# Performance work log

Hardware: AMD Instinct MI355X
Metric: run time of the kernel (lower is better)

## Reference

```python
import jax, jax.numpy as jnp
import numpy as np

N_KW, N_RT = 100000, 20000
D, H, O = 128, 128, 128
E_A, E_B, E_C = 1600000, 1600000, 320000


def setup_inputs() -> dict:
    key = jax.random.key(0)
    ks = jax.random.split(key, 32)
    inp = {
        "x_kw": jax.random.normal(ks[0], (N_KW, D), jnp.float32),
        "x_rt": jax.random.normal(ks[1], (N_RT, D), jnp.float32),
        "src_a": jax.random.randint(ks[2], (E_A,), 0, N_RT),
        "dst_a": jax.random.randint(ks[3], (E_A,), 0, N_KW),
        "src_b": jax.random.randint(ks[4], (E_B,), 0, N_KW),
        "dst_b": jax.random.randint(ks[5], (E_B,), 0, N_KW),
        "src_c": jax.random.randint(ks[6], (E_C,), 0, N_RT),
        "dst_c": jax.random.randint(ks[7], (E_C,), 0, N_RT),
    }
    # SAGEConv params per relation per layer: W_l (neighbor), b_l, W_r (root, no bias)
    i = 8
    dims = {1: (D, H), 2: (H, O)}
    for layer in (1, 2):
        din, dout = dims[layer]
        for rel in ("a", "b", "c"):
            inp[f"Wl{layer}{rel}"] = jax.random.normal(ks[i], (din, dout), jnp.float32) * 0.05; i += 1
            inp[f"bl{layer}{rel}"] = jnp.zeros((dout,), jnp.float32)
            inp[f"Wr{layer}{rel}"] = jax.random.normal(ks[i], (din, dout), jnp.float32) * 0.05; i += 1
    return inp


def _sage(x_src, x_dst, src, dst, Wl, bl, Wr):
    # PyG SAGEConv (mean aggr): lin_l(mean_j x_src[j]) + lin_r(x_dst)
    n = x_dst.shape[0]
    s = jax.ops.segment_sum(x_src[src], dst, num_segments=n)      # [n, din]
    cnt = jax.ops.segment_sum(jnp.ones_like(dst, dtype=x_src.dtype), dst, num_segments=n)
    mean = s / jnp.maximum(cnt, 1.0)[:, None]
    return mean @ Wl + bl + x_dst @ Wr


def reference(x_kw, x_rt, src_a, dst_a, src_b, dst_b, src_c, dst_c,
              Wl1a, bl1a, Wr1a, Wl1b, bl1b, Wr1b, Wl1c, bl1c, Wr1c,
              Wl2a, bl2a, Wr2a, Wl2b, bl2b, Wr2b, Wl2c, bl2c, Wr2c):
    # layer 1 (HeteroConv aggr='sum' over relations sharing a dst type)
    kw1 = (_sage(x_rt, x_kw, src_a, dst_a, Wl1a, bl1a, Wr1a)
           + _sage(x_kw, x_kw, src_b, dst_b, Wl1b, bl1b, Wr1b))
    rt1 = _sage(x_rt, x_rt, src_c, dst_c, Wl1c, bl1c, Wr1c)
    kw1 = jax.nn.relu(kw1)
    rt1 = jax.nn.relu(rt1)
    # layer 2
    kw2 = (_sage(rt1, kw1, src_a, dst_a, Wl2a, bl2a, Wr2a)
           + _sage(kw1, kw1, src_b, dst_b, Wl2b, bl2b, Wr2b))
    rt2 = _sage(rt1, rt1, src_c, dst_c, Wl2c, bl2c, Wr2c)
    return kw2, rt2
```

## Files before the change

### kernel.cpp

```cpp
#include <hip/hip_runtime.h>

typedef __attribute__((ext_vector_type(8))) short bf16x8;
typedef __attribute__((ext_vector_type(4))) float f32x4;
typedef __attribute__((ext_vector_type(2))) float f32x2;

static __device__ __forceinline__ unsigned short f2bf(float f) {
    unsigned int u = __float_as_uint(f);
    u += 0x7fffu + ((u >> 16) & 1u);
    return (unsigned short)(u >> 16);
}
static __device__ __forceinline__ float bf2f(unsigned short h) {
    return __uint_as_float(((unsigned int)h) << 16);
}

#define BSH 6
#define BUCKET 64
#define NBMAX 1600
#define CHSH 13


struct Rel {
    const int* src; const int* dst; int E; int nb; int Ndst;
    int hblk0, hnblk;
    int sblk0, snblk;
    int oblk0;
    int shift;
    int* bcnt; int* boff; int* bcur;
    unsigned* pairs; unsigned* ssrc; int* goff; float* invd;
};
struct Rels { Rel r[3]; };

struct PrepArgs {
    const float* W[10];
    const float* Wa[10];
    const float* b1a; const float* b1b; const float* b2a; const float* b2b;
};


__global__ void prep_hist_k(PrepArgs pa, unsigned short* __restrict__ Wt,
                            float* __restrict__ bc1, float* __restrict__ bc2,
                            Rels R, int prepBlocks) {
    int bid = blockIdx.x;
    if (bid < prepBlocks) {
        if (bid < 640) {
            int slot = bid >> 6;
            int i = ((bid & 63) << 8) + threadIdx.x;
            float v = pa.W[slot][i];
            const float* w2 = pa.Wa[slot];
            if (w2) v += w2[i];
            int k = i >> 7, n = i & 127;
            Wt[slot * 16384 + n * 128 + k] = f2bf(v);
        } else {
            int t = threadIdx.x;
            if (t < 128) bc1[t] = pa.b1a[t] + pa.b1b[t];
            else bc2[t - 128] = pa.b2a[t - 128] + pa.b2b[t - 128];
        }
        return;
    }
    int hb = bid - prepBlocks;
    const Rel* r;
    if (hb < R.r[1].hblk0) r = &R.r[0];
    else if (hb < R.r[2].hblk0) r = &R.r[1];
    else r = &R.r[2];
    __shared__ int h[NBMAX];
    for (int i = threadIdx.x; i < r->nb; i += 256) h[i] = 0;
    __syncthreads();
    for (int e = (hb - r->hblk0) * 256 + threadIdx.x; e < r->E; e += r->hnblk * 256)
        atomicAdd(&h[r->dst[e] >> BSH], 1);
    __syncthreads();
    for (int i = threadIdx.x; i < r->nb; i += 256)
        if (h[i]) atomicAdd(&r->bcnt[i], h[i]);
}


__global__ void bscan3_k(Rels R) {
    const Rel* r = &R.r[blockIdx.x];
    __shared__ int s[1024];
    int t = threadIdx.x;
    int nb = r->nb;
    int e0 = 2 * t, e1 = 2 * t + 1;
    int v0 = (e0 < nb) ? r->bcnt[e0] : 0;
    int v1 = (e1 < nb) ? r->bcnt[e1] : 0;
    s[t] = v0 + v1;
    __syncthreads();
    for (int o = 1; o < 1024; o <<= 1) {
        int x = (t >= o) ? s[t - o] : 0;
        __syncthreads();
        s[t] += x;
        __syncthreads();
    }
    int P = s[t] - (v0 + v1);
    if (e0 <= nb) { r->boff[e0] = P; if (e0 < nb) r->bcur[e0] = 0; }
    if (e1 <= nb) { r->boff[e1] = P + v0; if (e1 < nb) r->bcur[e1] = 0; }
}

__global__ __launch_bounds__(256) void bscatter3_k(Rels R) {
    const Rel* r;
    int bid = blockIdx.x;
    if (bid < R.r[1].sblk0) r = &R.r[0];
    else if (bid < R.r[2].sblk0) r = &R.r[1];
    else r = &R.r[2];
    __shared__ int h[NBMAX];
    __shared__ int base[NBMAX];
    int t = threadIdx.x;
    int nb = r->nb, E = r->E;
    for (int i = t; i < nb; i += 256) h[i] = 0;
    __syncthreads();
    int e0 = (bid - r->sblk0) * 8192;
    for (int i = 0; i < 32; i++) {
        int e = e0 + i * 256 + t;
        if (e < E) atomicAdd(&h[r->dst[e] >> BSH], 1);
    }
    __syncthreads();
    for (int i = t; i < nb; i += 256) {
        int c = h[i];
        base[i] = c ? (r->boff[i] + atomicAdd(&r->bcur[i], c)) : 0;
    }
    __syncthreads();
    for (int i = t; i < nb; i += 256) h[i] = 0;
    __syncthreads();
    for (int i = 0; i < 32; i++) {
        int e = e0 + i * 256 + t;
        if (e < E) {
            int d = r->dst[e];
            int b = d >> BSH;
            int pos = base[b] + atomicAdd(&h[b], 1);
            r->pairs[pos] = ((unsigned)(d & (BUCKET - 1)) << 17) | (unsigned)r->src[e];
        }
    }
}

static __device__ void sortb_body(const Rels& R, int bid) {
    const Rel* r;
    if (bid < R.r[1].oblk0) r = &R.r[0];
    else if (bid < R.r[2].oblk0) r = &R.r[1];
    else r = &R.r[2];
    int b = bid - r->oblk0;
    __shared__ int cnt[1024];
    __shared__ int sc[256];
    int t = threadIdx.x;
    for (int i = t; i < 1024; i += 256) cnt[i] = 0;
    __syncthreads();
    int j0 = r->boff[b], j1 = r->boff[b + 1];
    for (int j = j0 + t; j < j1; j += 256) {
        unsigned p = r->pairs[j];
        int d = (p >> 17) & 63;
        int ch = (int)((p & 0x1ffffu) >> CHSH); if (ch > 15) ch = 15;
        int bin = ((d & 7) << 7) | ((d >> 3) << 4) | ch;
        atomicAdd(&cnt[bin], 1);
    }
    __syncthreads();
    if (t < 64) {
        int b0 = ((t & 7) << 7) | ((t >> 3) << 4);
        int c = 0;
#pragma unroll
        for (int i = 0; i < 16; i++) c += cnt[b0 + i];
        int dd = (b << BSH) + t;
        if (dd < r->Ndst) r->invd[dd] = 1.f / (float)(c > 0 ? c : 1);
    }
    int c0 = cnt[4 * t], c1 = cnt[4 * t + 1], c2 = cnt[4 * t + 2], c3 = cnt[4 * t + 3];
    int tot = c0 + c1 + c2 + c3;
    sc[t] = tot;
    __syncthreads();
    for (int o = 1; o < 256; o <<= 1) {
        int x = (t >= o) ? sc[t - o] : 0;
        __syncthreads();
        sc[t] += x;
        __syncthreads();
    }
    int base = j0 + sc[t] - tot;
    if ((t & 3) == 0) r->goff[b * 64 + (t >> 2)] = base;
    cnt[4 * t] = base;
    cnt[4 * t + 1] = base + c0;
    cnt[4 * t + 2] = base + c0 + c1;
    cnt[4 * t + 3] = base + c0 + c1 + c2;
    if (t == 0 && b == r->nb - 1) r->goff[r->nb * 64] = r->E;
    __syncthreads();
    int shift = r->shift;
    for (int j = j0 + t; j < j1; j += 256) {
        unsigned p = r->pairs[j];
        int d = (p >> 17) & 63;
        int ch = (int)((p & 0x1ffffu) >> CHSH); if (ch > 15) ch = 15;
        int bin = ((d & 7) << 7) | ((d >> 3) << 4) | ch;
        int pos = atomicAdd(&cnt[bin], 1);
        r->ssrc[pos] = (p & 0x1ffffu) << shift;
    }
}


struct GemmJobs {
    const void* Akw; int Nkw;
    const unsigned short* Wk1; const float* bk; unsigned short* Zkw;
    const unsigned short* Wk2; unsigned char* Ckw8;
    const void* Art; int Nrt;
    const unsigned short* Wr1; const float* br; unsigned short* Zrt;
    const unsigned short* Wr2; unsigned short* Crt2;
    const unsigned short* Wr3; unsigned short* Crt3;
    int kwBlocks;
};

template <int AF32>
static __device__ void gemm_body(const GemmJobs& G, int bid) {
    bool iskw = bid < G.kwBlocks;
    const void* A = iskw ? G.Akw : G.Art;
    int N = iskw ? G.Nkw : G.Nrt;
    int lane = threadIdx.x & 63;
    int r16 = lane & 15, g = lane >> 4;
    int row0 = (iskw ? bid : bid - G.kwBlocks) * 64 + (threadIdx.x >> 6) * 16;
    int arow = row0 + r16;
    int arow_c = arow < N ? arow : N - 1;

    bf16x8 af[4];
    if (AF32) {
        const float* Af = (const float*)A + (size_t)arow_c * 128 + g * 8;
#pragma unroll
        for (int kc = 0; kc < 4; kc++) {
            float4 u0 = *(const float4*)(Af + kc * 32);
            float4 u1 = *(const float4*)(Af + kc * 32 + 4);
            bf16x8 rr;
            rr[0] = (short)f2bf(u0.x); rr[1] = (short)f2bf(u0.y);
            rr[2] = (short)f2bf(u0.z); rr[3] = (short)f2bf(u0.w);
            rr[4] = (short)f2bf(u1.x); rr[5] = (short)f2bf(u1.y);
            rr[6] = (short)f2bf(u1.z); rr[7] = (short)f2bf(u1.w);
            af[kc] = rr;
        }
    } else {
        const bf16x8* Ar = (const bf16x8*)((const unsigned short*)A + (size_t)arow_c * 128);
#pragma unroll
        for (int kc = 0; kc < 4; kc++) af[kc] = Ar[kc * 4 + g];
    }

    if (iskw) {
        f32x4 acc1[8], acc2[8];
#pragma unroll
        for (int ct = 0; ct < 8; ct++) { f32x4 z = {0.f,0.f,0.f,0.f}; acc1[ct] = z; acc2[ct] = z; }
#pragma unroll
        for (int kc = 0; kc < 4; kc++) {
#pragma unroll
            for (int ct = 0; ct < 8; ct++) {
                int wo = ((ct * 16 + r16) << 7) + kc * 32 + g * 8;
                bf16x8 b1 = *(const bf16x8*)(G.Wk1 + wo);
                acc1[ct] = __builtin_amdgcn_mfma_f32_16x16x32_bf16(af[kc], b1, acc1[ct], 0, 0, 0);
                bf16x8 b2 = *(const bf16x8*)(G.Wk2 + wo);
                acc2[ct] = __builtin_amdgcn_mfma_f32_16x16x32_bf16(af[kc], b2, acc2[ct], 0, 0, 0);
            }
        }
#pragma unroll
        for (int ct = 0; ct < 8; ct++) {
            int col = ct * 16 + r16;
            float bb = G.bk[col];
#pragma unroll
            for (int j = 0; j < 4; j++) {
                int r = row0 + g * 4 + j;
                if (r < N) {
                    G.Zkw[(size_t)r * 128 + col] = f2bf(acc1[ct][j] + bb);
                    float v2 = acc2[ct][j];
                    int pk = __builtin_amdgcn_cvt_pk_fp8_f32(v2, v2, 0, false);
                    G.Ckw8[(size_t)r * 128 + col] = (unsigned char)(pk & 0xff);
                }
            }
        }
    } else {
        f32x4 acc1[8], acc2[8], acc3[8];
#pragma unroll
        for (int ct = 0; ct < 8; ct++) {
            f32x4 z = {0.f,0.f,0.f,0.f}; acc1[ct] = z; acc2[ct] = z; acc3[ct] = z;
        }
#pragma unroll
        for (int kc = 0; kc < 4; kc++) {
#pragma unroll
            for (int ct = 0; ct < 8; ct++) {
                int wo = ((ct * 16 + r16) << 7) + kc * 32 + g * 8;
                bf16x8 b1 = *(const bf16x8*)(G.Wr1 + wo);
                acc1[ct] = __builtin_amdgcn_mfma_f32_16x16x32_bf16(af[kc], b1, acc1[ct], 0, 0, 0);
                bf16x8 b2 = *(const bf16x8*)(G.Wr2 + wo);
                acc2[ct] = __builtin_amdgcn_mfma_f32_16x16x32_bf16(af[kc], b2, acc2[ct], 0, 0, 0);
                bf16x8 b3 = *(const bf16x8*)(G.Wr3 + wo);
                acc3[ct] = __builtin_amdgcn_mfma_f32_16x16x32_bf16(af[kc], b3, acc3[ct], 0, 0, 0);
            }
        }
#pragma unroll
        for (int ct = 0; ct < 8; ct++) {
            int col = ct * 16 + r16;
            float bb = G.br[col];
#pragma unroll
            for (int j = 0; j < 4; j++) {
                int r = row0 + g * 4 + j;
                if (r < N) {
                    G.Zrt[(size_t)r * 128 + col] = f2bf(acc1[ct][j] + bb);
                    G.Crt2[(size_t)r * 128 + col] = f2bf(acc2[ct][j]);
                    G.Crt3[(size_t)r * 128 + col] = f2bf(acc3[ct][j]);
                }
            }
        }
    }
}

__global__ __launch_bounds__(256) void gemm_sort_k(GemmJobs G, Rels R, int gemmBlocks) {
    if ((int)blockIdx.x < gemmBlocks) gemm_body<1>(G, blockIdx.x);
    else sortb_body(R, blockIdx.x - gemmBlocks);
}

__global__ __launch_bounds__(256) void gemm_l2_k(GemmJobs G) {
    gemm_body<0>(G, blockIdx.x);
}

template <int FMT>
static __device__ __forceinline__ void agg_rel(float* acc, int b, int w, int h, int q,
                                               int dst0,
                                               const unsigned* __restrict__ sp,
                                               const int* __restrict__ goff,
                                               const float* __restrict__ invd,
                                               const char* __restrict__ Ybase) {
    int lanebyte = FMT ? (q << 2) : (q << 3);
#pragma unroll 1
    for (int r = 0; r < 8; r++) {
        int g = b * 64 + w * 8 + r;
        int jg0 = goff[g], jg1 = goff[g + 1];
        if (jg0 >= jg1) continue;
        int d = (r << 3) | w;
        f32x2 a01 = {0.f, 0.f}, a23 = {0.f, 0.f};
        int len = jg1 - jg0;
        int j = jg0;
        int jfull = jg0 + (len & ~15);
#pragma unroll 1
        for (; j < jfull; j += 16) {
            unsigned off[8];
#pragma unroll
            for (int k = 0; k < 8; k++) off[k] = sp[j + 2 * k + h];
            if (FMT == 0) {
                uint2 v[8];
#pragma unroll
                for (int k = 0; k < 8; k++)
                    v[k] = *(const uint2*)(Ybase + off[k] + lanebyte);
#pragma unroll
                for (int k = 0; k < 8; k++) {
                    f32x2 x01 = { __uint_as_float(v[k].x << 16),
                                  __uint_as_float(v[k].x & 0xffff0000u) };
                    f32x2 x23 = { __uint_as_float(v[k].y << 16),
                                  __uint_as_float(v[k].y & 0xffff0000u) };
                    a01 += x01;
                    a23 += x23;
                }
            } else {
                unsigned v[8];
#pragma unroll
                for (int k = 0; k < 8; k++)
                    v[k] = *(const unsigned*)(Ybase + off[k] + lanebyte);
#pragma unroll
                for (int k = 0; k < 8; k++) {
                    auto lo = __builtin_amdgcn_cvt_pk_f32_fp8(v[k], false);
                    auto hi = __builtin_amdgcn_cvt_pk_f32_fp8(v[k], true);
                    a01[0] += lo[0]; a01[1] += lo[1];
                    a23[0] += hi[0]; a23[1] += hi[1];
                }
            }
        }
        if (j < jg1) {
            if (FMT == 0) {
                uint2 v[8];
#pragma unroll
                for (int k = 0; k < 8; k++) {
                    int e = j + 2 * k + h;
                    int ec = e < jg1 ? e : jg1 - 1;
                    uint2 t2 = *(const uint2*)(Ybase + sp[ec] + lanebyte);
                    bool ok = e < jg1;
                    v[k].x = ok ? t2.x : 0u;
                    v[k].y = ok ? t2.y : 0u;
                }
#pragma unroll
                for (int k = 0; k < 8; k++) {
                    f32x2 x01 = { __uint_as_float(v[k].x << 16),
                                  __uint_as_float(v[k].x & 0xffff0000u) };
                    f32x2 x23 = { __uint_as_float(v[k].y << 16),
                                  __uint_as_float(v[k].y & 0xffff0000u) };
                    a01 += x01;
                    a23 += x23;
                }
            } else {
                unsigned v[8];
#pragma unroll
                for (int k = 0; k < 8; k++) {
                    int e = j + 2 * k + h;
                    int ec = e < jg1 ? e : jg1 - 1;
                    unsigned tv = *(const unsigned*)(Ybase + sp[ec] + lanebyte);
                    v[k] = (e < jg1) ? tv : 0u;
                }
#pragma unroll
                for (int k = 0; k < 8; k++) {
                    auto lo = __builtin_amdgcn_cvt_pk_f32_fp8(v[k], false);
                    auto hi = __builtin_amdgcn_cvt_pk_f32_fp8(v[k], true);
                    a01[0] += lo[0]; a01[1] += lo[1];
                    a23[0] += hi[0]; a23[1] += hi[1];
                }
            }
        }
        a01[0] += __shfl_xor(a01[0], 32);
        a01[1] += __shfl_xor(a01[1], 32);
        a23[0] += __shfl_xor(a23[0], 32);
        a23[1] += __shfl_xor(a23[1], 32);
        float inv = invd[dst0 + d];
        float v0 = (h ? a23[0] : a01[0]) * inv;
        float v1 = (h ? a23[1] : a01[1]) * inv;
        int ba = d * 128 + q + h * 64;
        acc[ba] += v0;
        acc[ba + 32] += v1;
    }
}

struct AggJob {
    const unsigned short* Zin; int Ndst;
    const unsigned* sp0; const int* goff0; const float* invd0; const void* Y0; int fmt0;
    const unsigned* sp1; const int* goff1; const float* invd1; const void* Y1; int fmt1;
    int nrel;
    float* OutF; unsigned short* OutB;
};

template <int RELU, int OUTBF16>
__global__ __launch_bounds__(512) void bagg2_k(AggJob JK, AggJob JR, int kwBlocks) {
    __shared__ float acc[BUCKET * 128];
    bool iskw = blockIdx.x < (unsigned)kwBlocks;
    AggJob J = iskw ? JK : JR;
    int b = iskw ? blockIdx.x : blockIdx.x - kwBlocks;
    int t = threadIdx.x;
    int dst0 = b << BSH;
    int nrow = J.Ndst - dst0; if (nrow > BUCKET) nrow = BUCKET;

    for (int c = t; c < BUCKET * 32; c += 512) {
        int r = c >> 5, m = c & 31;
        float z0 = 0.f, z1 = 0.f, z2 = 0.f, z3 = 0.f;
        if (r < nrow) {
            ushort4 z = *(const ushort4*)(J.Zin + (size_t)(dst0 + r) * 128 + (m << 2));
            z0 = bf2f(z.x); z1 = bf2f(z.y); z2 = bf2f(z.z); z3 = bf2f(z.w);
        }
        acc[r * 128 + m] = z0;
        acc[r * 128 + 32 + m] = z1;
        acc[r * 128 + 64 + m] = z2;
        acc[r * 128 + 96 + m] = z3;
    }
    __syncthreads();

    int w = t >> 6, lane = t & 63;
    int h = lane >> 5, q = lane & 31;
    if (J.fmt0 == 0) agg_rel<0>(acc, b, w, h, q, dst0, J.sp0, J.goff0, J.invd0, (const char*)J.Y0);
    else agg_rel<1>(acc, b, w, h, q, dst0, J.sp0, J.goff0, J.invd0, (const char*)J.Y0);
    if (J.nrel == 2) {
        if (J.fmt1 == 0) agg_rel<0>(acc, b, w, h, q, dst0, J.sp1, J.goff1, J.invd1, (const char*)J.Y1);
        else agg_rel<1>(acc, b, w, h, q, dst0, J.sp1, J.goff1, J.invd1, (const char*)J.Y1);
    }
    __syncthreads();
    for (int c = t; c < BUCKET * 32; c += 512) {
        int r = c >> 5, m = c & 31;
        if (r < nrow) {
            float x0 = acc[r * 128 + m];
            float x1 = acc[r * 128 + 32 + m];
            float x2 = acc[r * 128 + 64 + m];
            float x3 = acc[r * 128 + 96 + m];
            if (RELU) {
                x0 = fmaxf(x0, 0.f); x1 = fmaxf(x1, 0.f);
                x2 = fmaxf(x2, 0.f); x3 = fmaxf(x3, 0.f);
            }
            size_t o = (size_t)(dst0 + r) * 128 + (m << 2);
            if (OUTBF16) {
                ushort4 ov;
                ov.x = f2bf(x0); ov.y = f2bf(x1); ov.z = f2bf(x2); ov.w = f2bf(x3);
                *(ushort4*)(J.OutB + o) = ov;
            } else {
                *(float4*)(J.OutF + o) = make_float4(x0, x1, x2, x3);
            }
        }
    }
}


static inline size_t align256(size_t x) { return (x + 255) & ~size_t(255); }

extern "C" void kernel_launch(void* const* d_in, const int* in_sizes, int n_in,
                              void* d_out, int out_size, void* d_ws, size_t ws_size,
                              hipStream_t stream) {
    const float* x_kw = (const float*)d_in[0];
    const float* x_rt = (const float*)d_in[1];
    const int* src_a = (const int*)d_in[2];
    const int* dst_a = (const int*)d_in[3];
    const int* src_b = (const int*)d_in[4];
    const int* dst_b = (const int*)d_in[5];
    const int* src_c = (const int*)d_in[6];
    const int* dst_c = (const int*)d_in[7];
    const float *Wl1a = (const float*)d_in[8],  *bl1a = (const float*)d_in[9],  *Wr1a = (const float*)d_in[10];
    const float *Wl1b = (const float*)d_in[11], *bl1b = (const float*)d_in[12], *Wr1b = (const float*)d_in[13];
    const float *Wl1c = (const float*)d_in[14], *bl1c = (const float*)d_in[15], *Wr1c = (const float*)d_in[16];
    const float *Wl2a = (const float*)d_in[17], *bl2a = (const float*)d_in[18], *Wr2a = (const float*)d_in[19];
    const float *Wl2b = (const float*)d_in[20], *bl2b = (const float*)d_in[21], *Wr2b = (const float*)d_in[22];
    const float *Wl2c = (const float*)d_in[23], *bl2c = (const float*)d_in[24], *Wr2c = (const float*)d_in[25];

    const int NKW = in_sizes[0] / 128;
    const int NRT = in_sizes[1] / 128;
    const int EA = in_sizes[2], EB = in_sizes[4], EC = in_sizes[6];
    const int nb_kw = (NKW + BUCKET - 1) / BUCKET;
    const int nb_rt = (NRT + BUCKET - 1) / BUCKET;

    char* ws = (char*)d_ws;
    size_t off = 0;
    auto alloc = [&](size_t bytes) -> char* {
        off = align256(off);
        char* p = ws + off;
        off += bytes;
        return p;
    };
    unsigned short* Wt = (unsigned short*)alloc(10 * 16384 * 2);
    float* bc1 = (float*)alloc(128 * 4);
    float* bc2 = (float*)alloc(128 * 4);
    int* bcnt3 = (int*)alloc(3 * NBMAX * 4);
    int* bcur3 = (int*)alloc(3 * NBMAX * 4);
    int* boff_a = (int*)alloc((NBMAX + 1) * 4);
    int* boff_b = (int*)alloc((NBMAX + 1) * 4);
    int* boff_c = (int*)alloc((NBMAX + 1) * 4);
    int* goff_a = (int*)alloc(((size_t)nb_kw * 64 + 1) * 4);
    int* goff_b = (int*)alloc(((size_t)nb_kw * 64 + 1) * 4);
    int* goff_c = (int*)alloc(((size_t)nb_rt * 64 + 1) * 4);
    float* invd_a = (float*)alloc((size_t)NKW * 4);
    float* invd_b = (float*)alloc((size_t)NKW * 4);
    float* invd_c = (float*)alloc((size_t)NRT * 4);
    unsigned* pairs_a = (unsigned*)alloc((size_t)EA * 4);
    unsigned* pairs_b = (unsigned*)alloc((size_t)EB * 4);
    unsigned* pairs_c = (unsigned*)alloc((size_t)EC * 4);
    unsigned* sp_a = (unsigned*)alloc((size_t)EA * 4);
    unsigned* sp_b = (unsigned*)alloc((size_t)EB * 4);
    unsigned* sp_c = (unsigned*)alloc((size_t)EC * 4);
    unsigned short* Ya = (unsigned short*)alloc((size_t)NRT * 128 * 2);
    unsigned char*  Yb = (unsigned char*)alloc((size_t)NKW * 128);
    unsigned short* Yc = (unsigned short*)alloc((size_t)NRT * 128 * 2);
    unsigned short* Zkw = (unsigned short*)alloc((size_t)NKW * 128 * 2);
    unsigned short* Zrt = (unsigned short*)alloc((size_t)NRT * 128 * 2);
    unsigned short* kw1_bf = (unsigned short*)alloc((size_t)NKW * 128 * 2);
    unsigned short* rt1_bf = (unsigned short*)alloc((size_t)NRT * 128 * 2);
    (void)ws_size;

    float* out_kw = (float*)d_out;
    float* out_rt = out_kw + (size_t)NKW * 128;

    Rels R;
    int hA = 128, hB = 128, hC = 64;
    int sA = (EA + 8191) / 8192, sB = (EB + 8191) / 8192, sC = (EC + 8191) / 8192;
    R.r[0] = {src_a, dst_a, EA, nb_kw, NKW, 0, hA, 0, sA, 0, 8,
              bcnt3, boff_a, bcur3, pairs_a, sp_a, goff_a, invd_a};
    R.r[1] = {src_b, dst_b, EB, nb_kw, NKW, hA, hB, sA, sB, nb_kw, 7,
              bcnt3 + NBMAX, boff_b, bcur3 + NBMAX, pairs_b, sp_b, goff_b, invd_b};
    R.r[2] = {src_c, dst_c, EC, nb_rt, NRT, hA + hB, hC, sA + sB, sC, 2 * nb_kw, 8,
              bcnt3 + 2 * NBMAX, boff_c, bcur3 + 2 * NBMAX, pairs_c, sp_c, goff_c, invd_c};

    hipMemsetAsync(bcnt3, 0, 3 * NBMAX * 4, stream);
    PrepArgs pa;
    pa.W[0] = Wr1a; pa.Wa[0] = Wr1b;
    pa.W[1] = Wl1a; pa.Wa[1] = nullptr;
    pa.W[2] = Wl1b; pa.Wa[2] = nullptr;
    pa.W[3] = Wl1c; pa.Wa[3] = nullptr;
    pa.W[4] = Wr1c; pa.Wa[4] = nullptr;
    pa.W[5] = Wr2a; pa.Wa[5] = Wr2b;
    pa.W[6] = Wl2a; pa.Wa[6] = nullptr;
    pa.W[7] = Wl2b; pa.Wa[7] = nullptr;
    pa.W[8] = Wl2c; pa.Wa[8] = nullptr;
    pa.W[9] = Wr2c; pa.Wa[9] = nullptr;
    pa.b1a = bl1a; pa.b1b = bl1b; pa.b2a = bl2a; pa.b2b = bl2b;
    prep_hist_k<<<641 + hA + hB + hC, 256, 0, stream>>>(pa, Wt, bc1, bc2, R, 641);
    unsigned short* W0 = Wt + 0 * 16384;
    unsigned short* W1 = Wt + 1 * 16384;
    unsigned short* W2 = Wt + 2 * 16384;
    unsigned short* W3 = Wt + 3 * 16384;
    unsigned short* W4 = Wt + 4 * 16384;
    unsigned short* W5 = Wt + 5 * 16384;
    unsigned short* W6 = Wt + 6 * 16384;
    unsigned short* W7 = Wt + 7 * 16384;
    unsigned short* W8 = Wt + 8 * 16384;
    unsigned short* W9 = Wt + 9 * 16384;

    bscan3_k<<<3, 1024, 0, stream>>>(R);
    bscatter3_k<<<sA + sB + sC, 256, 0, stream>>>(R);

    const int kwB = (NKW + 63) / 64, rtB = (NRT + 63) / 64;
    const int nsort = 2 * nb_kw + nb_rt;

    GemmJobs G1;
    G1.Akw = x_kw; G1.Nkw = NKW; G1.Wk1 = W0; G1.bk = bc1; G1.Zkw = Zkw; G1.Wk2 = W2; G1.Ckw8 = Yb;
    G1.Art = x_rt; G1.Nrt = NRT; G1.Wr1 = W4; G1.br = bl1c; G1.Zrt = Zrt;
    G1.Wr2 = W1; G1.Crt2 = Ya; G1.Wr3 = W3; G1.Crt3 = Yc;
    G1.kwBlocks = kwB;
    gemm_sort_k<<<kwB + rtB + nsort, 256, 0, stream>>>(G1, R, kwB + rtB);

    AggJob JK1 = {Zkw, NKW, sp_a, goff_a, invd_a, Ya, 0, sp_b, goff_b, invd_b, Yb, 1, 2,
                  nullptr, kw1_bf};
    AggJob JR1 = {Zrt, NRT, sp_c, goff_c, invd_c, Yc, 0, nullptr, nullptr, nullptr, nullptr, 0, 1,
                  nullptr, rt1_bf};
    bagg2_k<1, 1><<<nb_kw + nb_rt, 512, 0, stream>>>(JK1, JR1, nb_kw);

    GemmJobs G2;
    G2.Akw = kw1_bf; G2.Nkw = NKW; G2.Wk1 = W5; G2.bk = bc2; G2.Zkw = Zkw; G2.Wk2 = W7; G2.Ckw8 = Yb;
    G2.Art = rt1_bf; G2.Nrt = NRT; G2.Wr1 = W9; G2.br = bl2c; G2.Zrt = Zrt;
    G2.Wr2 = W6; G2.Crt2 = Ya; G2.Wr3 = W8; G2.Crt3 = Yc;
    G2.kwBlocks = kwB;
    gemm_l2_k<<<kwB + rtB, 256, 0, stream>>>(G2);

    AggJob JK2 = {Zkw, NKW, sp_a, goff_a, invd_a, Ya, 0, sp_b, goff_b, invd_b, Yb, 1, 2,
                  out_kw, nullptr};
    AggJob JR2 = {Zrt, NRT, sp_c, goff_c, invd_c, Yc, 0, nullptr, nullptr, nullptr, nullptr, 0, 1,
                  out_rt, nullptr};
    bagg2_k<0, 0><<<nb_kw + nb_rt, 512, 0, stream>>>(JK2, JR2, nb_kw);
}
```

Before: 595.8 us.

## Gather wider per-lane rows with 4 edges per wave-step and bpermute indices

Reworks the gather-aggregation inner loop so each wave handles 4 edges at once with 16 lanes per edge. Each lane loads 16-byte (bf16) or 8-byte (fp8) vectors instead of 8 or 4 bytes. Edge source offsets are loaded once per 32 edges with one coalesced read and spread across lanes with ds_bpermute, replacing redundant per-lane index loads. The price is a two-level cross-lane reduction (xor 16 and 32) over 8 accumulators and extra permute instructions; tail handling now masks loads per edge.

Result: slower. 669.8 us (+12.4%).

```diff
diff --git a/kernel.cpp b/kernel.cpp
--- a/kernel.cpp
+++ b/kernel.cpp
@@ -306,105 +306,126 @@
 }
 
 template <int FMT>
-static __device__ __forceinline__ void agg_rel(float* acc, int b, int w, int h, int q,
+static __device__ __forceinline__ void agg_rel(float* acc, int b, int w, int lane,
                                                int dst0,
                                                const unsigned* __restrict__ sp,
                                                const int* __restrict__ goff,
                                                const float* __restrict__ invd,
                                                const char* __restrict__ Ybase) {
-    int lanebyte = FMT ? (q << 2) : (q << 3);
+    int g = lane >> 4, q = lane & 15;
+    int lb = FMT ? (q << 3) : (q << 4);
+    int idx0 = (0 + g) << 2, idx1 = (4 + g) << 2, idx2 = (8 + g) << 2, idx3 = (12 + g) << 2;
+    int loc0 = (((2 * g) & 3) << 5) + 2 * q + (g >> 1);
+    int loc1 = (((2 * g + 1) & 3) << 5) + 2 * q + (g >> 1);
 #pragma unroll 1
     for (int r = 0; r < 8; r++) {
-        int g = b * 64 + w * 8 + r;
-        int jg0 = goff[g], jg1 = goff[g + 1];
+        int gi = b * 64 + w * 8 + r;
+        int jg0 = goff[gi], jg1 = goff[gi + 1];
         if (jg0 >= jg1) continue;
         int d = (r << 3) | w;
-        f32x2 a01 = {0.f, 0.f}, a23 = {0.f, 0.f};
-        int len = jg1 - jg0;
-        int j = jg0;
-        int jfull = jg0 + (len & ~15);
+        f32x2 a01 = {0.f, 0.f}, a23 = {0.f, 0.f}, a45 = {0.f, 0.f}, a67 = {0.f, 0.f};
 #pragma unroll 1
-        for (; j < jfull; j += 16) {
-            unsigned off[8];
-#pragma unroll
-            for (int k = 0; k < 8; k++) off[k] = sp[j + 2 * k + h];
-            if (FMT == 0) {
-                uint2 v[8];
-#pragma unroll
-                for (int k = 0; k < 8; k++)
-                    v[k] = *(const uint2*)(Ybase + off[k] + lanebyte);
-#pragma unroll
-                for (int k = 0; k < 8; k++) {
-                    f32x2 x01 = { __uint_as_float(v[k].x << 16),
-                                  __uint_as_float(v[k].x & 0xffff0000u) };
-                    f32x2 x23 = { __uint_as_float(v[k].y << 16),
-                                  __uint_as_float(v[k].y & 0xffff0000u) };
-                    a01 += x01;
-                    a23 += x23;
+        for (int jb = jg0; jb < jg1; jb += 32) {
+            int ji = jb + (lane & 31);
+            ji = ji < jg1 ? ji : jg1 - 1;
+            int spv = (int)sp[ji];
+            if (jb + 32 <= jg1) {
+#pragma unroll
+                for (int hb = 0; hb < 2; hb++) {
+                    int hofs = hb << 6;
+                    unsigned o0 = (unsigned)__builtin_amdgcn_ds_bpermute(idx0 + hofs, spv);
+                    unsigned o1 = (unsigned)__builtin_amdgcn_ds_bpermute(idx1 + hofs, spv);
+                    unsigned o2 = (unsigned)__builtin_amdgcn_ds_bpermute(idx2 + hofs, spv);
+                    unsigned o3 = (unsigned)__builtin_amdgcn_ds_bpermute(idx3 + hofs, spv);
+                    if (FMT == 0) {
+                        uint4 v0 = *(const uint4*)(Ybase + o0 + lb);
+                        uint4 v1 = *(const uint4*)(Ybase + o1 + lb);
+                        uint4 v2 = *(const uint4*)(Ybase + o2 + lb);
+                        uint4 v3 = *(const uint4*)(Ybase + o3 + lb);
+#pragma unroll
+                        for (int k = 0; k < 4; k++) {
+                            uint4 v = k == 0 ? v0 : k == 1 ? v1 : k == 2 ? v2 : v3;
+                            f32x2 x0 = { __uint_as_float(v.x << 16), __uint_as_float(v.x & 0xffff0000u) };
+                            f32x2 x1 = { __uint_as_float(v.y << 16), __uint_as_float(v.y & 0xffff0000u) };
+                            f32x2 x2 = { __uint_as_float(v.z << 16), __uint_as_float(v.z & 0xffff0000u) };
+                            f32x2 x3 = { __uint_as_float(v.w << 16), __uint_as_float(v.w & 0xffff0000u) };
+                            a01 += x0; a23 += x1; a45 += x2; a67 += x3;
+                        }
+                    } else {
+                        uint2 v0 = *(const uint2*)(Ybase + o0 + lb);
+                        uint2 v1 = *(const uint2*)(Ybase + o1 + lb);
+                        uint2 v2 = *(const uint2*)(Ybase + o2 + lb);
+                        uint2 v3 = *(const uint2*)(Ybase + o3 + lb);
+#pragma unroll
+                        for (int k = 0; k < 4; k++) {
+                            uint2 v = k == 0 ? v0 : k == 1 ? v1 : k == 2 ? v2 : v3;
+                            auto l0 = __builtin_amdgcn_cvt_pk_f32_fp8(v.x, false);
+                            auto h0 = __builtin_amdgcn_cvt_pk_f32_fp8(v.x, true);
+                            auto l1 = __builtin_amdgcn_cvt_pk_f32_fp8(v.y, false);
+                            auto h1 = __builtin_amdgcn_cvt_pk_f32_fp8(v.y, true);
+                            a01[0] += l0[0]; a01[1] += l0[1];
+                            a23[0] += h0[0]; a23[1] += h0[1];
+                            a45[0] += l1[0]; a45[1] += l1[1];
+                            a67[0] += h1[0]; a67[1] += h1[1];
+                        }
+                    }
                 }
             } else {
-                unsigned v[8];
-#pragma unroll
-                for (int k = 0; k < 8; k++)
-                    v[k] = *(const unsigned*)(Ybase + off[k] + lanebyte);
-#pragma unroll
-                for (int k = 0; k < 8; k++) {
-                    auto lo = __builtin_amdgcn_cvt_pk_f32_fp8(v[k], false);
-                    auto hi = __builtin_amdgcn_cvt_pk_f32_fp8(v[k], true);
-                    a01[0] += lo[0]; a01[1] += lo[1];
-                    a23[0] += hi[0]; a23[1] += hi[1];
+#pragma unroll
+                for (int hb = 0; hb < 2; hb++) {
+                    int ebase = jb + (hb << 4) + g;
+                    if (ebase >= jg1 && g == 0) {}
+                    if (jb + (hb << 4) >= jg1) break;
+                    int hofs = hb << 6;
+                    unsigned o0 = (unsigned)__builtin_amdgcn_ds_bpermute(idx0 + hofs, spv);
+                    unsigned o1 = (unsigned)__builtin_amdgcn_ds_bpermute(idx1 + hofs, spv);
+                    unsigned o2 = (unsigned)__builtin_amdgcn_ds_bpermute(idx2 + hofs, spv);
+                    unsigned o3 = (unsigned)__builtin_amdgcn_ds_bpermute(idx3 + hofs, spv);
+#pragma unroll
+                    for (int k = 0; k < 4; k++) {
+                        unsigned ok = k == 0 ? o0 : k == 1 ? o1 : k == 2 ? o2 : o3;
+                        bool live = (jb + (hb << 4) + 4 * k + g) < jg1;
+                        if (FMT == 0) {
+                            uint4 v = *(const uint4*)(Ybase + ok + lb);
+                            unsigned vx = live ? v.x : 0u, vy = live ? v.y : 0u;
+                            unsigned vz = live ? v.z : 0u, vw = live ? v.w : 0u;
+                            f32x2 x0 = { __uint_as_float(vx << 16), __uint_as_float(vx & 0xffff0000u) };
+                            f32x2 x1 = { __uint_as_float(vy << 16), __uint_as_float(vy & 0xffff0000u) };
+                            f32x2 x2 = { __uint_as_float(vz << 16), __uint_as_float(vz & 0xffff0000u) };
+                            f32x2 x3 = { __uint_as_float(vw << 16), __uint_as_float(vw & 0xffff0000u) };
+                            a01 += x0; a23 += x1; a45 += x2; a67 += x3;
+                        } else {
+                            uint2 v = *(const uint2*)(Ybase + ok + lb);
+                            unsigned vx = live ? v.x : 0u, vy = live ? v.y : 0u;
+                            auto l0 = __builtin_amdgcn_cvt_pk_f32_fp8(vx, false);
+                            auto h0 = __builtin_amdgcn_cvt_pk_f32_fp8(vx, true);
+                            auto l1 = __builtin_amdgcn_cvt_pk_f32_fp8(vy, false);
+                            auto h1 = __builtin_amdgcn_cvt_pk_f32_fp8(vy, true);
+                            a01[0] += l0[0]; a01[1] += l0[1];
+                            a23[0] += h0[0]; a23[1] += h0[1];
+                            a45[0] += l1[0]; a45[1] += l1[1];
+                            a67[0] += h1[0]; a67[1] += h1[1];
+                        }
+                    }
                 }
             }
         }
-        if (j < jg1) {
-            if (FMT == 0) {
-                uint2 v[8];
-#pragma unroll
-                for (int k = 0; k < 8; k++) {
-                    int e = j + 2 * k + h;
-                    int ec = e < jg1 ? e : jg1 - 1;
-                    uint2 t2 = *(const uint2*)(Ybase + sp[ec] + lanebyte);
-                    bool ok = e < jg1;
-                    v[k].x = ok ? t2.x : 0u;
-                    v[k].y = ok ? t2.y : 0u;
-                }
-#pragma unroll
-                for (int k = 0; k < 8; k++) {
-                    f32x2 x01 = { __uint_as_float(v[k].x << 16),
-                                  __uint_as_float(v[k].x & 0xffff0000u) };
-                    f32x2 x23 = { __uint_as_float(v[k].y << 16),
-                                  __uint_as_float(v[k].y & 0xffff0000u) };
-                    a01 += x01;
-                    a23 += x23;
-                }
-            } else {
-                unsigned v[8];
-#pragma unroll
-                for (int k = 0; k < 8; k++) {
-                    int e = j + 2 * k + h;
-                    int ec = e < jg1 ? e : jg1 - 1;
-                    unsigned tv = *(const unsigned*)(Ybase + sp[ec] + lanebyte);
-                    v[k] = (e < jg1) ? tv : 0u;
-                }
-#pragma unroll
-                for (int k = 0; k < 8; k++) {
-                    auto lo = __builtin_amdgcn_cvt_pk_f32_fp8(v[k], false);
-                    auto hi = __builtin_amdgcn_cvt_pk_f32_fp8(v[k], true);
-                    a01[0] += lo[0]; a01[1] += lo[1];
-                    a23[0] += hi[0]; a23[1] += hi[1];
-                }
-            }
-        }
-        a01[0] += __shfl_xor(a01[0], 32);
-        a01[1] += __shfl_xor(a01[1], 32);
-        a23[0] += __shfl_xor(a23[0], 32);
-        a23[1] += __shfl_xor(a23[1], 32);
+        float s0 = a01[0], s1 = a01[1], s2 = a23[0], s3 = a23[1];
+        float s4 = a45[0], s5 = a45[1], s6 = a67[0], s7 = a67[1];
+        s0 += __shfl_xor(s0, 16); s0 += __shfl_xor(s0, 32);
+        s1 += __shfl_xor(s1, 16); s1 += __shfl_xor(s1, 32);
+        s2 += __shfl_xor(s2, 16); s2 += __shfl_xor(s2, 32);
+        s3 += __shfl_xor(s3, 16); s3 += __shfl_xor(s3, 32);
+        s4 += __shfl_xor(s4, 16); s4 += __shfl_xor(s4, 32);
+        s5 += __shfl_xor(s5, 16); s5 += __shfl_xor(s5, 32);
+        s6 += __shfl_xor(s6, 16); s6 += __shfl_xor(s6, 32);
+        s7 += __shfl_xor(s7, 16); s7 += __shfl_xor(s7, 32);
+        float w0 = g == 0 ? s0 : g == 1 ? s2 : g == 2 ? s4 : s6;
+        float w1 = g == 0 ? s1 : g == 1 ? s3 : g == 2 ? s5 : s7;
         float inv = invd[dst0 + d];
-        float v0 = (h ? a23[0] : a01[0]) * inv;
-        float v1 = (h ? a23[1] : a01[1]) * inv;
-        int ba = d * 128 + q + h * 64;
-        acc[ba] += v0;
-        acc[ba + 32] += v1;
+        int ba = d * 128;
+        acc[ba + loc0] += w0 * inv;
+        acc[ba + loc1] += w1 * inv;
     }
 }
 
@@ -441,12 +462,11 @@
     __syncthreads();
 
     int w = t >> 6, lane = t & 63;
-    int h = lane >> 5, q = lane & 31;
-    if (J.fmt0 == 0) agg_rel<0>(acc, b, w, h, q, dst0, J.sp0, J.goff0, J.invd0, (const char*)J.Y0);
-    else agg_rel<1>(acc, b, w, h, q, dst0, J.sp0, J.goff0, J.invd0, (const char*)J.Y0);
+    if (J.fmt0 == 0) agg_rel<0>(acc, b, w, lane, dst0, J.sp0, J.goff0, J.invd0, (const char*)J.Y0);
+    else agg_rel<1>(acc, b, w, lane, dst0, J.sp0, J.goff0, J.invd0, (const char*)J.Y0);
     if (J.nrel == 2) {
-        if (J.fmt1 == 0) agg_rel<0>(acc, b, w, h, q, dst0, J.sp1, J.goff1, J.invd1, (const char*)J.Y1);
-        else agg_rel<1>(acc, b, w, h, q, dst0, J.sp1, J.goff1, J.invd1, (const char*)J.Y1);
+        if (J.fmt1 == 0) agg_rel<0>(acc, b, w, lane, dst0, J.sp1, J.goff1, J.invd1, (const char*)J.Y1);
+        else agg_rel<1>(acc, b, w, lane, dst0, J.sp1, J.goff1, J.invd1, (const char*)J.Y1);
     }
     __syncthreads();
     for (int c = t; c < BUCKET * 32; c += 512) {
```
